# Optimization experiments

Hardware: AMD Instinct MI355X
Metric: run time of the kernel (lower is better)

The kernel has to match this reference:

```python
import jax, jax.numpy as jnp
import numpy as np

H = 512          # hidden_size
B, S, L = 32, 2048, 2
D = 2 * H        # encoder output / hidden feature dim


def setup_inputs() -> dict:
    key = jax.random.key(0)
    ks = jax.random.split(key, 9)
    lim1 = 1.0 / np.sqrt(D)
    limv = 1.0 / np.sqrt(H)
    return {
        "hidden": jax.random.normal(ks[0], (L, B, D), jnp.float32),
        "encoder_outputs": jax.random.normal(ks[1], (B, S, D), jnp.float32),
        "mask": jax.random.randint(ks[2], (B, S), 0, 2, jnp.int32),
        "W1_w": jax.random.uniform(ks[3], (H, D), jnp.float32, -lim1, lim1),
        "W1_b": jax.random.uniform(ks[4], (H,), jnp.float32, -lim1, lim1),
        "W2_w": jax.random.uniform(ks[5], (H, D), jnp.float32, -lim1, lim1),
        "W2_b": jax.random.uniform(ks[6], (H,), jnp.float32, -lim1, lim1),
        "V_w": jax.random.uniform(ks[7], (1, H), jnp.float32, -limv, limv),
        "V_b": jax.random.uniform(ks[8], (1,), jnp.float32, -limv, limv),
    }


def reference(hidden, encoder_outputs, mask, W1_w, W1_b, W2_w, W2_b, V_w, V_b):
    # query: last layer hidden state, broadcast over sequence -> [B, 1, D]
    query = hidden[-1][:, None, :]
    # W1(enc) + W2(query): [B, S, H]
    proj = (jnp.einsum('bsd,hd->bsh', encoder_outputs, W1_w) + W1_b
            + jnp.einsum('bqd,hd->bqh', query, W2_w) + W2_b)
    # V projection -> scores [B, S]
    score = jnp.einsum('bsh,h->bs', jnp.tanh(proj), V_w[0]) + V_b[0]
    score = jnp.where(mask == 0, jnp.float32(-1e9), score)
    attn_weights = jax.nn.softmax(score, axis=1)          # [B, S]
    context = jnp.einsum('bs,bsd->bd', attn_weights, encoder_outputs)  # [B, D]
    return context, attn_weights
```

## Files before the change

### kernel.cpp

```cpp
#include <hip/hip_runtime.h>
#include <hip/hip_bf16.h>

#define B_ 32
#define S_ 2048
#define D_ 1024
#define H_ 512
#define M_ (B_*S_)
#define BM 128
#define BN 128
#define BK 64
#define TILE (BM*BK)

typedef __attribute__((ext_vector_type(8))) short short8;
typedef __attribute__((ext_vector_type(4))) float f32x4;

__device__ __forceinline__ unsigned short f2bf(float f){
  return __builtin_bit_cast(unsigned short, __float2bfloat16(f));
}

__device__ __forceinline__ float fast_tanh(float x){
  return 1.f - 2.f*__builtin_amdgcn_rcpf(__expf(2.f*x) + 1.f);
}

__device__ __forceinline__ int swz(int row, int kshort){
  return row*BK + ((kshort & 56) ^ ((row&7)<<3)) + (kshort & 7);
}

__global__ __launch_bounds__(256) void convw_kernel(
    const float* __restrict__ W1, unsigned short* __restrict__ W1s){
  int tid = blockIdx.x*256 + threadIdx.x;
  int n = tid*8;
  int h = n >> 10;
  int k = n & 1023;
  int bn = h >> 7, row = h & 127;
  int kt = k >> 6, kk = k & 63;
  float4 lo = *(const float4*)(W1 + n);
  float4 hi = *(const float4*)(W1 + n + 4);
  short8 r;
  r[0]=(short)f2bf(lo.x); r[1]=(short)f2bf(lo.y); r[2]=(short)f2bf(lo.z); r[3]=(short)f2bf(lo.w);
  r[4]=(short)f2bf(hi.x); r[5]=(short)f2bf(hi.y); r[6]=(short)f2bf(hi.z); r[7]=(short)f2bf(hi.w);
  *(short8*)&W1s[(bn*16 + kt)*TILE + swz(row, kk)] = r;
}

__global__ __launch_bounds__(256) void qbias_kernel(
    const float* __restrict__ hidden, const float* __restrict__ W2,
    const float* __restrict__ W1b, const float* __restrict__ W2b,
    float* __restrict__ qb){
  int b = blockIdx.x, h0 = blockIdx.y*64;
  int wave = threadIdx.x>>6, lane = threadIdx.x&63;
  const float* q = hidden + (size_t)(B_ + b)*D_;
  for (int i=0;i<16;i++){
    int h = h0 + wave*16 + i;
    const float* w = W2 + (size_t)h*D_;
    float s = 0.f;
    #pragma unroll
    for (int it=0; it<4; ++it){
      int d = it*256 + lane*4;
      const float4 qq = *(const float4*)(q+d);
      const float4 ww = *(const float4*)(w+d);
      s += qq.x*ww.x + qq.y*ww.y + qq.z*ww.z + qq.w*ww.w;
    }
    #pragma unroll
    for (int off=1; off<64; off<<=1) s += __shfl_xor(s, off);
    if (lane==0) qb[b*H_ + h] = s + W1b[h] + W2b[h];
  }
}

__global__ __launch_bounds__(256, 3) void score_gemm(
    const float* __restrict__ enc, const unsigned short* __restrict__ W1s,
    const float* __restrict__ qb, const float* __restrict__ Vw,
    float* __restrict__ score_p){
  const int id  = blockIdx.x;
  const int xcd = id & 7;
  const int j   = id >> 3;
  const int bm  = xcd*64 + (j >> 2);
  const int bn  = j & 3;
  const int m0 = bm*BM, h0 = bn*BN;
  const int tid = threadIdx.x, lane = tid&63, wave = tid>>6;
  const int wm = (wave>>1)*64, wn = (wave&1)*64;

  __shared__ __align__(16) unsigned short As[TILE];
  __shared__ __align__(16) unsigned short Bs[2][TILE];

  f32x4 acc[4][4];
  #pragma unroll
  for (int i=0;i<4;i++)
    #pragma unroll
    for (int j2=0;j2<4;j2++)
      acc[i][j2] = (f32x4)(0.f);

  float4 aLo[4], aHi[4];

#define LOAD_A(KT) do{ const int kkx=(KT)*BK; \
  _Pragma("unroll") for (int i=0;i<4;i++){ \
    int c=tid+i*256; int row=c>>3, kc=(c&7)*8; \
    const float4* pa=(const float4*)(enc+(size_t)(m0+row)*D_+kkx+kc); \
    aLo[i]=pa[0]; aHi[i]=pa[1]; } }while(0)

#define GLD_B(KT,P) do{ const unsigned short* bsrc=W1s+(size_t)(bn*16+(KT))*TILE; \
  _Pragma("unroll") for (int i=0;i<4;i++){ \
    __builtin_amdgcn_global_load_lds( \
      (const __attribute__((address_space(1))) unsigned int*)(bsrc+i*2048+tid*8), \
      (__attribute__((address_space(3))) unsigned int*)&Bs[P][i*2048+tid*8], 16,0,0); } }while(0)

#define CVT_A() do{ \
  _Pragma("unroll") for (int i=0;i<4;i++){ \
    int c=tid+i*256; int row=c>>3, kc=(c&7)*8; short8 av; \
    av[0]=(short)f2bf(aLo[i].x); av[1]=(short)f2bf(aLo[i].y); \
    av[2]=(short)f2bf(aLo[i].z); av[3]=(short)f2bf(aLo[i].w); \
    av[4]=(short)f2bf(aHi[i].x); av[5]=(short)f2bf(aHi[i].y); \
    av[6]=(short)f2bf(aHi[i].z); av[7]=(short)f2bf(aHi[i].w); \
    *(short8*)&As[swz(row,kc)] = av; } }while(0)

#define COMPUTE(P) do{ \
  _Pragma("unroll") for (int kh=0; kh<2; ++kh){ \
    const int kb = kh*32 + (lane>>4)*8; \
    short8 af[4], bf[4]; \
    _Pragma("unroll") for (int mi=0;mi<4;mi++){ \
      int row=wm+mi*16+(lane&15); af[mi]=*(const short8*)&As[swz(row,kb)]; } \
    _Pragma("unroll") for (int ni=0;ni<4;ni++){ \
      int row=wn+ni*16+(lane&15); bf[ni]=*(const short8*)&Bs[P][swz(row,kb)]; } \
    _Pragma("unroll") for (int mi=0;mi<4;mi++) \
      _Pragma("unroll") for (int ni=0;ni<4;ni++) \
        acc[mi][ni]=__builtin_amdgcn_mfma_f32_16x16x32_bf16(af[mi],bf[ni],acc[mi][ni],0,0,0); \
  } }while(0)

  LOAD_A(0);
  GLD_B(0,0);
  CVT_A();
  LOAD_A(1);
  GLD_B(1,1);
  asm volatile("s_waitcnt vmcnt(12) lgkmcnt(0)" ::: "memory");
  __builtin_amdgcn_s_barrier();

  #pragma unroll 2
  for (int kt=0; kt<14; ++kt){
    const int p = kt&1;
    COMPUTE(p);
    __builtin_amdgcn_s_barrier();
    GLD_B(kt+2, p);
    CVT_A();
    LOAD_A(kt+2);
    asm volatile("s_waitcnt lgkmcnt(0)" ::: "memory");
    __builtin_amdgcn_s_barrier();
  }
  COMPUTE(0);
  __builtin_amdgcn_s_barrier();
  CVT_A();
  asm volatile("s_waitcnt lgkmcnt(0)" ::: "memory");
  __builtin_amdgcn_s_barrier();
  COMPUTE(1);

  const int bidx = m0 >> 11;
  float qv[4], vwv[4];
  #pragma unroll
  for (int ni=0;ni<4;ni++){
    int h = h0 + wn + ni*16 + (lane&15);
    qv[ni]  = qb[bidx*H_ + h];
    vwv[ni] = Vw[h];
  }
  __shared__ float psum[4][BM];
  #pragma unroll
  for (int mi=0;mi<4;mi++){
    #pragma unroll
    for (int r=0;r<4;r++){
      float s = 0.f;
      #pragma unroll
      for (int ni=0;ni<4;ni++) s += fast_tanh(acc[mi][ni][r] + qv[ni]) * vwv[ni];
      s += __shfl_xor(s,1); s += __shfl_xor(s,2);
      s += __shfl_xor(s,4); s += __shfl_xor(s,8);
      if ((lane&15)==0){
        int m = wm + mi*16 + ((lane>>4)<<2) + r;
        psum[wave][m] = s;
      }
    }
  }
  __syncthreads();
  if (tid < BM){
    int w0 = (tid>>6)*2;
    score_p[(size_t)bn*M_ + m0 + tid] = psum[w0][tid] + psum[w0+1][tid];
  }
}

__global__ __launch_bounds__(256) void softmax_kernel(
    const float* __restrict__ score_p, const int* __restrict__ mask,
    float* __restrict__ attn){
  int b = blockIdx.x, tid = threadIdx.x;
  int wave = tid>>6, lane = tid&63;
  __shared__ float red[8];
  float v[8];
  float mx = -1e30f;
  #pragma unroll
  for (int i=0;i<8;i++){
    int idx = b*S_ + tid + i*256;
    float sc = score_p[idx] + score_p[M_+idx] + score_p[2*M_+idx] + score_p[3*M_+idx];
    v[i] = (mask[idx]==0) ? -1e9f : sc;
    mx = fmaxf(mx, v[i]);
  }
  #pragma unroll
  for (int off=1; off<64; off<<=1) mx = fmaxf(mx, __shfl_xor(mx, off));
  if (lane==0) red[wave] = mx;
  __syncthreads();
  mx = fmaxf(fmaxf(red[0],red[1]), fmaxf(red[2],red[3]));
  float sum = 0.f;
  #pragma unroll
  for (int i=0;i<8;i++){ v[i] = __expf(v[i]-mx); sum += v[i]; }
  #pragma unroll
  for (int off=1; off<64; off<<=1) sum += __shfl_xor(sum, off);
  if (lane==0) red[4+wave] = sum;
  __syncthreads();
  float inv = 1.f/(red[4]+red[5]+red[6]+red[7]);
  #pragma unroll
  for (int i=0;i<8;i++) attn[b*S_ + tid + i*256] = v[i]*inv;
}

__global__ __launch_bounds__(256) void context_part(
    const float* __restrict__ enc, const float* __restrict__ attn,
    float* __restrict__ ctx_p){
  int b = blockIdx.x, sc = blockIdx.y;
  int s0 = sc*64;
  int d4 = threadIdx.x*4;
  const float* ep = enc + ((size_t)b*S_ + s0)*D_ + d4;
  const float* ap = attn + b*S_ + s0;
  float4 a0 = make_float4(0.f,0.f,0.f,0.f);
  float4 a1 = make_float4(0.f,0.f,0.f,0.f);
  #pragma unroll 4
  for (int i=0;i<64;i+=2){
    float w0 = ap[i], w1 = ap[i+1];
    float4 e0 = *(const float4*)(ep + (size_t)i*D_);
    float4 e1 = *(const float4*)(ep + (size_t)(i+1)*D_);
    a0.x = fmaf(w0, e0.x, a0.x); a0.y = fmaf(w0, e0.y, a0.y);
    a0.z = fmaf(w0, e0.z, a0.z); a0.w = fmaf(w0, e0.w, a0.w);
    a1.x = fmaf(w1, e1.x, a1.x); a1.y = fmaf(w1, e1.y, a1.y);
    a1.z = fmaf(w1, e1.z, a1.z); a1.w = fmaf(w1, e1.w, a1.w);
  }
  float4 t = make_float4(a0.x+a1.x, a0.y+a1.y, a0.z+a1.z, a0.w+a1.w);
  *(float4*)(ctx_p + ((size_t)b*32 + sc)*D_ + d4) = t;
}

__global__ __launch_bounds__(256) void context_reduce(
    const float* __restrict__ ctx_p, float* __restrict__ ctx){
  int b = blockIdx.x;
  int d4 = threadIdx.x*4;
  f32x4 s = (f32x4)(0.f);
  #pragma unroll 8
  for (int sc=0; sc<32; ++sc)
    s += *(const f32x4*)(ctx_p + ((size_t)b*32 + sc)*D_ + d4);
  *(f32x4*)(ctx + (size_t)b*D_ + d4) = s;
}

extern "C" void kernel_launch(void* const* d_in, const int* in_sizes, int n_in,
                              void* d_out, int out_size, void* d_ws, size_t ws_size,
                              hipStream_t stream){
  const float* hidden = (const float*)d_in[0];
  const float* enc    = (const float*)d_in[1];
  const int*   mask   = (const int*)d_in[2];
  const float* W1w    = (const float*)d_in[3];
  const float* W1b    = (const float*)d_in[4];
  const float* W2w    = (const float*)d_in[5];
  const float* W2b    = (const float*)d_in[6];
  const float* Vw     = (const float*)d_in[7];
  float* out = (float*)d_out;

  float* qb           = (float*)d_ws;
  float* score_p      = qb + B_*H_;
  unsigned short* W1s = (unsigned short*)(score_p + 4*M_);
  float* ctx_p        = (float*)(W1s + H_*D_);

  convw_kernel  <<<H_*D_/8/256,     256, 0, stream>>>(W1w, W1s);
  qbias_kernel  <<<dim3(B_, H_/64), 256, 0, stream>>>(hidden, W2w, W1b, W2b, qb);
  score_gemm    <<<4*(M_/BM),       256, 0, stream>>>(enc, W1s, qb, Vw, score_p);
  softmax_kernel<<<B_,              256, 0, stream>>>(score_p, mask, out + B_*D_);
  context_part  <<<dim3(B_, 32),    256, 0, stream>>>(enc, out + B_*D_, ctx_p);
  context_reduce<<<B_,              256, 0, stream>>>(ctx_p, out);
}
```

Baseline: 176.7 us.

## Double-buffer A register prefetch to deepen global load pipeline

Adds a second set of register buffers for the fp32 encoder tile, so A loads are issued two k-steps ahead instead of one. Scheduling barriers pin the order of loads and conversions, and the vmcnt waits are loosened so more memory traffic stays in flight across compute. The loop is restructured with a different prologue and epilogue. In exchange it uses 32 more VGPRs per thread, which may lower occupancy or cause spills, and the hand-tuned waitcnt values must match the issue order exactly.

```diff
diff --git a/kernel.cpp b/kernel.cpp
--- a/kernel.cpp
+++ b/kernel.cpp
@@ -89,13 +89,18 @@
     for (int j2=0;j2<4;j2++)
       acc[i][j2] = (f32x4)(0.f);
 
-  float4 aLo[4], aHi[4];
-
-#define LOAD_A(KT) do{ const int kkx=(KT)*BK; \
+  float4 aLo0[4], aHi0[4], aLo1[4], aHi1[4];
+
+#define LOAD_A0(KT) do{ const int kkx=(KT)*BK; \
   _Pragma("unroll") for (int i=0;i<4;i++){ \
     int c=tid+i*256; int row=c>>3, kc=(c&7)*8; \
     const float4* pa=(const float4*)(enc+(size_t)(m0+row)*D_+kkx+kc); \
-    aLo[i]=pa[0]; aHi[i]=pa[1]; } }while(0)
+    aLo0[i]=pa[0]; aHi0[i]=pa[1]; } }while(0)
+#define LOAD_A1(KT) do{ const int kkx=(KT)*BK; \
+  _Pragma("unroll") for (int i=0;i<4;i++){ \
+    int c=tid+i*256; int row=c>>3, kc=(c&7)*8; \
+    const float4* pa=(const float4*)(enc+(size_t)(m0+row)*D_+kkx+kc); \
+    aLo1[i]=pa[0]; aHi1[i]=pa[1]; } }while(0)
 
 #define GLD_B(KT,P) do{ const unsigned short* bsrc=W1s+(size_t)(bn*16+(KT))*TILE; \
   _Pragma("unroll") for (int i=0;i<4;i++){ \
@@ -103,13 +108,21 @@
       (const __attribute__((address_space(1))) unsigned int*)(bsrc+i*2048+tid*8), \
       (__attribute__((address_space(3))) unsigned int*)&Bs[P][i*2048+tid*8], 16,0,0); } }while(0)
 
-#define CVT_A() do{ \
+#define CVT_A0() do{ \
   _Pragma("unroll") for (int i=0;i<4;i++){ \
     int c=tid+i*256; int row=c>>3, kc=(c&7)*8; short8 av; \
-    av[0]=(short)f2bf(aLo[i].x); av[1]=(short)f2bf(aLo[i].y); \
-    av[2]=(short)f2bf(aLo[i].z); av[3]=(short)f2bf(aLo[i].w); \
-    av[4]=(short)f2bf(aHi[i].x); av[5]=(short)f2bf(aHi[i].y); \
-    av[6]=(short)f2bf(aHi[i].z); av[7]=(short)f2bf(aHi[i].w); \
+    av[0]=(short)f2bf(aLo0[i].x); av[1]=(short)f2bf(aLo0[i].y); \
+    av[2]=(short)f2bf(aLo0[i].z); av[3]=(short)f2bf(aLo0[i].w); \
+    av[4]=(short)f2bf(aHi0[i].x); av[5]=(short)f2bf(aHi0[i].y); \
+    av[6]=(short)f2bf(aHi0[i].z); av[7]=(short)f2bf(aHi0[i].w); \
+    *(short8*)&As[swz(row,kc)] = av; } }while(0)
+#define CVT_A1() do{ \
+  _Pragma("unroll") for (int i=0;i<4;i++){ \
+    int c=tid+i*256; int row=c>>3, kc=(c&7)*8; short8 av; \
+    av[0]=(short)f2bf(aLo1[i].x); av[1]=(short)f2bf(aLo1[i].y); \
+    av[2]=(short)f2bf(aLo1[i].z); av[3]=(short)f2bf(aLo1[i].w); \
+    av[4]=(short)f2bf(aHi1[i].x); av[5]=(short)f2bf(aHi1[i].y); \
+    av[6]=(short)f2bf(aHi1[i].z); av[7]=(short)f2bf(aHi1[i].w); \
     *(short8*)&As[swz(row,kc)] = av; } }while(0)
 
 #define COMPUTE(P) do{ \
@@ -125,29 +138,40 @@
         acc[mi][ni]=__builtin_amdgcn_mfma_f32_16x16x32_bf16(af[mi],bf[ni],acc[mi][ni],0,0,0); \
   } }while(0)
 
-  LOAD_A(0);
-  GLD_B(0,0);
-  CVT_A();
-  LOAD_A(1);
-  GLD_B(1,1);
-  asm volatile("s_waitcnt vmcnt(12) lgkmcnt(0)" ::: "memory");
-  __builtin_amdgcn_s_barrier();
-
-  #pragma unroll 2
-  for (int kt=0; kt<14; ++kt){
+#define SB() __builtin_amdgcn_sched_barrier(0)
+
+  GLD_B(0,0);  SB();
+  LOAD_A0(0);  SB();
+  GLD_B(1,1);  SB();
+  LOAD_A1(1);  SB();
+  CVT_A0();
+  LOAD_A0(2);  SB();
+  asm volatile("s_waitcnt lgkmcnt(0)" ::: "memory");
+  __builtin_amdgcn_s_barrier();
+
+  for (int kt=0; kt<13; ++kt){
     const int p = kt&1;
     COMPUTE(p);
     __builtin_amdgcn_s_barrier();
-    GLD_B(kt+2, p);
-    CVT_A();
-    LOAD_A(kt+2);
-    asm volatile("s_waitcnt lgkmcnt(0)" ::: "memory");
+    GLD_B(kt+2, p);  SB();
+    if ((kt+1)&1) CVT_A1(); else CVT_A0();
+    if ((kt+3)&1) LOAD_A1(kt+3); else LOAD_A0(kt+3);
+    SB();
+    asm volatile("s_waitcnt vmcnt(20) lgkmcnt(0)" ::: "memory");
     __builtin_amdgcn_s_barrier();
   }
+  COMPUTE(1);
+  __builtin_amdgcn_s_barrier();
+  GLD_B(15,1);  SB();
+  CVT_A0();
+  SB();
+  asm volatile("s_waitcnt vmcnt(12) lgkmcnt(0)" ::: "memory");
+  __builtin_amdgcn_s_barrier();
   COMPUTE(0);
   __builtin_amdgcn_s_barrier();
-  CVT_A();
-  asm volatile("s_waitcnt lgkmcnt(0)" ::: "memory");
+  CVT_A1();
+  SB();
+  asm volatile("s_waitcnt vmcnt(0) lgkmcnt(0)" ::: "memory");
   __builtin_amdgcn_s_barrier();
   COMPUTE(1);
 
```

Result: slower. 256.8 us (+45.3%).

## Restructure score GEMM main loop into a single-barrier, triple-buffered software pipeline

Applied to the files above, without the earlier changes.

The score GEMM K-loop is rewritten so that A is double-buffered and B is triple-buffered in LDS. Each step issues the next B async load and A conversion/store, then runs the MFMA compute with only one wait+barrier per iteration instead of two, and sched_barriers pin the instruction order. The psum scratch now reuses the A buffer. The aim is to overlap global loads, conversion and MFMA while cutting barrier stalls, at the cost of more LDS, which drops the occupancy hint from 3 to 2 blocks per CU.

```diff
diff --git a/kernel.cpp b/kernel.cpp
--- a/kernel.cpp
+++ b/kernel.cpp
@@ -66,7 +66,7 @@
   }
 }
 
-__global__ __launch_bounds__(256, 3) void score_gemm(
+__global__ __launch_bounds__(256, 2) void score_gemm(
     const float* __restrict__ enc, const unsigned short* __restrict__ W1s,
     const float* __restrict__ qb, const float* __restrict__ Vw,
     float* __restrict__ score_p){
@@ -79,8 +79,8 @@
   const int tid = threadIdx.x, lane = tid&63, wave = tid>>6;
   const int wm = (wave>>1)*64, wn = (wave&1)*64;
 
-  __shared__ __align__(16) unsigned short As[TILE];
-  __shared__ __align__(16) unsigned short Bs[2][TILE];
+  __shared__ __align__(16) unsigned short As[2][TILE];
+  __shared__ __align__(16) unsigned short Bs[3][TILE];
 
   f32x4 acc[4][4];
   #pragma unroll
@@ -103,21 +103,21 @@
       (const __attribute__((address_space(1))) unsigned int*)(bsrc+i*2048+tid*8), \
       (__attribute__((address_space(3))) unsigned int*)&Bs[P][i*2048+tid*8], 16,0,0); } }while(0)
 
-#define CVT_A() do{ \
+#define CVT_A(QW) do{ \
   _Pragma("unroll") for (int i=0;i<4;i++){ \
     int c=tid+i*256; int row=c>>3, kc=(c&7)*8; short8 av; \
     av[0]=(short)f2bf(aLo[i].x); av[1]=(short)f2bf(aLo[i].y); \
     av[2]=(short)f2bf(aLo[i].z); av[3]=(short)f2bf(aLo[i].w); \
     av[4]=(short)f2bf(aHi[i].x); av[5]=(short)f2bf(aHi[i].y); \
     av[6]=(short)f2bf(aHi[i].z); av[7]=(short)f2bf(aHi[i].w); \
-    *(short8*)&As[swz(row,kc)] = av; } }while(0)
-
-#define COMPUTE(P) do{ \
+    *(short8*)&As[QW][swz(row,kc)] = av; } }while(0)
+
+#define COMPUTE(Q,P) do{ \
   _Pragma("unroll") for (int kh=0; kh<2; ++kh){ \
     const int kb = kh*32 + (lane>>4)*8; \
     short8 af[4], bf[4]; \
     _Pragma("unroll") for (int mi=0;mi<4;mi++){ \
-      int row=wm+mi*16+(lane&15); af[mi]=*(const short8*)&As[swz(row,kb)]; } \
+      int row=wm+mi*16+(lane&15); af[mi]=*(const short8*)&As[Q][swz(row,kb)]; } \
     _Pragma("unroll") for (int ni=0;ni<4;ni++){ \
       int row=wn+ni*16+(lane&15); bf[ni]=*(const short8*)&Bs[P][swz(row,kb)]; } \
     _Pragma("unroll") for (int mi=0;mi<4;mi++) \
@@ -125,31 +125,43 @@
         acc[mi][ni]=__builtin_amdgcn_mfma_f32_16x16x32_bf16(af[mi],bf[ni],acc[mi][ni],0,0,0); \
   } }while(0)
 
-  LOAD_A(0);
-  GLD_B(0,0);
-  CVT_A();
-  LOAD_A(1);
-  GLD_B(1,1);
-  asm volatile("s_waitcnt vmcnt(12) lgkmcnt(0)" ::: "memory");
-  __builtin_amdgcn_s_barrier();
-
-  #pragma unroll 2
-  for (int kt=0; kt<14; ++kt){
-    const int p = kt&1;
-    COMPUTE(p);
-    __builtin_amdgcn_s_barrier();
-    GLD_B(kt+2, p);
-    CVT_A();
-    LOAD_A(kt+2);
-    asm volatile("s_waitcnt lgkmcnt(0)" ::: "memory");
-    __builtin_amdgcn_s_barrier();
-  }
-  COMPUTE(0);
-  __builtin_amdgcn_s_barrier();
-  CVT_A();
-  asm volatile("s_waitcnt lgkmcnt(0)" ::: "memory");
-  __builtin_amdgcn_s_barrier();
-  COMPUTE(1);
+#define SB() __builtin_amdgcn_sched_barrier(0)
+#define WAITV_BAR(N) do{ \
+  asm volatile("s_waitcnt vmcnt(" #N ") lgkmcnt(0)" ::: "memory"); \
+  __builtin_amdgcn_s_barrier(); }while(0)
+
+#define STEP(KT, S2, QW, QR, PR) do{ \
+  GLD_B((KT)+2, S2);  SB(); \
+  CVT_A(QW);           \
+  LOAD_A((KT)+2);     SB(); \
+  COMPUTE(QR, PR); \
+  WAITV_BAR(12); }while(0)
+
+  GLD_B(0,0);  SB();
+  LOAD_A(0);   SB();
+  CVT_A(0);
+  GLD_B(1,1);  SB();
+  LOAD_A(1);   SB();
+  WAITV_BAR(12);
+
+  STEP(0,  2, 1, 0, 0);
+  STEP(1,  0, 0, 1, 1);
+  STEP(2,  1, 1, 0, 2);
+  STEP(3,  2, 0, 1, 0);
+  STEP(4,  0, 1, 0, 1);
+  STEP(5,  1, 0, 1, 2);
+  STEP(6,  2, 1, 0, 0);
+  STEP(7,  0, 0, 1, 1);
+  STEP(8,  1, 1, 0, 2);
+  STEP(9,  2, 0, 1, 0);
+  STEP(10, 0, 1, 0, 1);
+  STEP(11, 1, 0, 1, 2);
+  STEP(12, 2, 1, 0, 0);
+  STEP(13, 0, 0, 1, 1);
+  CVT_A(1);
+  COMPUTE(0, 2);
+  WAITV_BAR(0);
+  COMPUTE(1, 0);
 
   const int bidx = m0 >> 11;
   float qv[4], vwv[4];
@@ -159,7 +171,8 @@
     qv[ni]  = qb[bidx*H_ + h];
     vwv[ni] = Vw[h];
   }
-  __shared__ float psum[4][BM];
+  __builtin_amdgcn_s_barrier();
+  float* psum = (float*)&As[0][0];
   #pragma unroll
   for (int mi=0;mi<4;mi++){
     #pragma unroll
@@ -171,14 +184,14 @@
       s += __shfl_xor(s,4); s += __shfl_xor(s,8);
       if ((lane&15)==0){
         int m = wm + mi*16 + ((lane>>4)<<2) + r;
-        psum[wave][m] = s;
+        psum[wave*BM + m] = s;
       }
     }
   }
   __syncthreads();
   if (tid < BM){
     int w0 = (tid>>6)*2;
-    score_p[(size_t)bn*M_ + m0 + tid] = psum[w0][tid] + psum[w0+1][tid];
+    score_p[(size_t)bn*M_ + m0 + tid] = psum[w0*BM + tid] + psum[(w0+1)*BM + tid];
   }
 }
 
```

Result: faster. 171.0 us, median of 2 (-3.2%).
